# Optimization experiments

Hardware: AMD Instinct MI355X
Metric: run time of the kernel (lower is better)

## Reference

```python
import jax, jax.numpy as jnp
import numpy as np

EMBED_DIM = 512
B, N = 8, 2048


def setup_inputs() -> dict:
    key = jax.random.key(0)
    ks = jax.random.split(key, 9)
    d = EMBED_DIM
    s = 1.0 / np.sqrt(d)
    return {
        "x": jax.random.normal(ks[0], (B, N, d), dtype=jnp.float32),
        "Wq": jax.random.uniform(ks[1], (d, d), jnp.float32, -s, s),
        "bq": jax.random.uniform(ks[2], (d,), jnp.float32, -s, s),
        "Wk": jax.random.uniform(ks[3], (d, d), jnp.float32, -s, s),
        "bk": jax.random.uniform(ks[4], (d,), jnp.float32, -s, s),
        "Wv": jax.random.uniform(ks[5], (d, d), jnp.float32, -s, s),
        "bv": jax.random.uniform(ks[6], (d,), jnp.float32, -s, s),
        "Wo": jax.random.uniform(ks[7], (d, d), jnp.float32, -s, s),
        "bo": jax.random.uniform(ks[8], (d,), jnp.float32, -s, s),
    }


def reference(x, Wq, bq, Wk, bk, Wv, bv, Wo, bo):
    d = x.shape[-1]
    scale = d ** (-0.5)
    q = x @ Wq + bq              # [B, N, D]
    k = x @ Wk + bk
    v = x @ Wv + bv
    attn = jnp.einsum('bnd,bmd->bnm', q, k) * scale  # [B, N, N]
    attn = jax.nn.softmax(attn, axis=-1)
    out = jnp.einsum('bnm,bmd->bnd', attn, v)
    return out @ Wo + bo
```

## Files before the change

### kernel.cpp

```cpp
#include <hip/hip_runtime.h>
#include <hip/hip_bf16.h>
#include <hip/hip_fp8.h>
#include <stdint.h>

typedef __bf16 bf16;
typedef __attribute__((ext_vector_type(8))) short short8;
typedef __attribute__((ext_vector_type(4))) float f32x4;
typedef __attribute__((ext_vector_type(4))) bf16 bf16x4;
typedef __attribute__((ext_vector_type(8))) int int8v;
typedef __attribute__((ext_vector_type(4))) int int4v;

#define DIM 512
#define NBATCH 8
#define SEQ 2048

__device__ __forceinline__ void gld_lds16(const void* g, void* l) {
    __builtin_amdgcn_global_load_lds(
        (const __attribute__((address_space(1))) void*)g,
        (__attribute__((address_space(3))) void*)l,
        16, 0, 0);
}

__device__ __forceinline__ unsigned char f32_to_e4m3(float v) {
#if __has_builtin(__builtin_amdgcn_cvt_pk_fp8_f32)
    return (unsigned char)(__builtin_amdgcn_cvt_pk_fp8_f32(v, v, 0, false) & 0xff);
#else
    return __hip_cvt_float_to_fp8(v, __HIP_SATFINITE, __HIP_E4M3);
#endif
}

template <int MODE, int SWIZ>
__global__ __launch_bounds__(256) void gemm_bt(
    const bf16* __restrict__ A, const bf16* __restrict__ Bt,
    void* __restrict__ Cv, uint8_t* __restrict__ Vt,
    const float* __restrict__ bias, int N, int K, int gx)
{
    __shared__ bf16 smem[32768];
    bf16* Asb = smem;
    bf16* Bsb = smem + 16384;

    int bx, by;
    {
        const unsigned g = blockIdx.x;
        const unsigned xcd = g & 7;
        const unsigned t = g >> 3;
        const unsigned per = (gridDim.x >> 3) / (unsigned)gx;
        by = xcd * per + t / (unsigned)gx;
        bx = t % (unsigned)gx;
    }

    const int tid  = threadIdx.x;
    const int lane = tid & 63;
    const int w    = tid >> 6;
    const int wr   = w >> 1;
    const int wc   = w & 1;
    const int lm   = lane & 15;
    const int lk   = lane >> 4;
    const int fs   = lm & 7;
    const int rq   = tid >> 3;
    const int pc   = tid & 7;
    const int scol = ((pc ^ (rq & 7)) * 8);

    const bf16* Ag = A + (size_t)(by * 128) * K;
    const bf16* Bg = Bt + (size_t)(bx * 128) * K;

    f32x4 acc[4][4];
#pragma unroll
    for (int i = 0; i < 4; ++i)
#pragma unroll
        for (int j = 0; j < 4; ++j)
            acc[i][j] = (f32x4){0.f, 0.f, 0.f, 0.f};

    auto stage = [&](int kb, int buf) {
#pragma unroll
        for (int t = 0; t < 4; ++t) {
            const int r = t * 32 + rq;
            gld_lds16(Ag + (size_t)r * K + kb + scol,
                      Asb + buf * 8192 + t * 2048 + tid * 8);
            gld_lds16(Bg + (size_t)r * K + kb + scol,
                      Bsb + buf * 8192 + t * 2048 + tid * 8);
        }
    };
    auto compute = [&](int buf) {
        const bf16* Ab = Asb + buf * 8192;
        const bf16* Bb = Bsb + buf * 8192;
#pragma unroll
        for (int s = 0; s < 2; ++s) {
            const int u = ((s * 4 + lk) ^ fs) * 8;
            short8 fa[4], fb[4];
#pragma unroll
            for (int i = 0; i < 4; ++i)
                fa[i] = *(const short8*)&Ab[(wr * 64 + i * 16 + lm) * 64 + u];
#pragma unroll
            for (int j = 0; j < 4; ++j)
                fb[j] = *(const short8*)&Bb[(wc * 64 + j * 16 + lm) * 64 + u];
#pragma unroll
            for (int i = 0; i < 4; ++i)
#pragma unroll
                for (int j = 0; j < 4; ++j)
                    acc[i][j] = __builtin_amdgcn_mfma_f32_16x16x32_bf16(
                        fa[i], fb[j], acc[i][j], 0, 0, 0);
        }
    };

    stage(0, 0);
    __syncthreads();
    const int E = K >> 6;
#pragma unroll 2
    for (int e = 0; e < E; ++e) {
        if (e + 1 < E) stage((e + 1) << 6, (e + 1) & 1);
        compute(e & 1);
        __syncthreads();
    }

#pragma unroll
    for (int i = 0; i < 4; ++i)
#pragma unroll
        for (int j = 0; j < 4; ++j) {
            const int col = bx * 128 + wc * 64 + j * 16 + lm;
            const float bv = bias[col];
#pragma unroll
            for (int r = 0; r < 4; ++r)
                acc[i][j][r] += bv;
        }

    if (MODE == 2) {
        float* ft = (float*)smem;
        float* outp = (float*)Cv;
#pragma unroll
        for (int h = 0; h < 2; ++h) {
            if (wr == h) {
#pragma unroll
                for (int i = 0; i < 4; ++i)
#pragma unroll
                    for (int j = 0; j < 4; ++j)
#pragma unroll
                        for (int r = 0; r < 4; ++r)
                            ft[(i * 16 + lk * 4 + r) * 132 + wc * 64 + j * 16 + lm] =
                                acc[i][j][r];
            }
            __syncthreads();
            const int rr = tid >> 5, cc = (tid & 31) * 4;
#pragma unroll
            for (int p = 0; p < 8; ++p) {
                const int row = p * 8 + rr;
                *(float4*)&outp[(size_t)(by * 128 + h * 64 + row) * N +
                                bx * 128 + cc] = *(const float4*)&ft[row * 132 + cc];
            }
            __syncthreads();
        }
        return;
    }

    const int sub  = (bx * 128) >> 9;
    const int col0 = (bx * 128) & 511;

    if (sub == 2) {
        const int b  = (by * 128) >> 11;
        const int n0 = (by * 128) & 2047;
        uint8_t* t8 = (uint8_t*)smem;
#pragma unroll
        for (int i = 0; i < 4; ++i)
#pragma unroll
            for (int j = 0; j < 4; ++j)
#pragma unroll
                for (int r = 0; r < 4; ++r) {
                    const int fl = wc * 64 + j * 16 + lm;
                    const int nl = wr * 64 + i * 16 + lk * 4 + r;
                    t8[fl * 144 + nl] = f32_to_e4m3(32.0f * acc[i][j][r]);
                }
        __syncthreads();
        const int f = tid >> 1, nh = (tid & 1) * 64;
#pragma unroll
        for (int p = 0; p < 4; ++p) {
            const uint4 raw = *(const uint4*)&t8[f * 144 + nh + p * 16];
            *(uint4*)&Vt[((size_t)(b * 512 + col0 + f)) * 2048 +
                         n0 + nh + p * 16] = raw;
        }
        return;
    }

    uint8_t* d8 = (uint8_t*)Cv + (size_t)sub * 8388608;
    uint8_t* t8 = (uint8_t*)smem;
#pragma unroll
    for (int h = 0; h < 2; ++h) {
        if (wr == h) {
#pragma unroll
            for (int i = 0; i < 4; ++i)
#pragma unroll
                for (int j = 0; j < 4; ++j)
#pragma unroll
                    for (int r = 0; r < 4; ++r)
                        t8[(i * 16 + lk * 4 + r) * 144 + wc * 64 + j * 16 + lm] =
                            f32_to_e4m3(32.0f * acc[i][j][r]);
        }
        __syncthreads();
        const int rr = tid >> 3, cc = (tid & 7) * 16;
#pragma unroll
        for (int p = 0; p < 2; ++p) {
            const int row = p * 32 + rr;
            const uint4 raw = *(const uint4*)&t8[row * 144 + cc];
            *(uint4*)&d8[(size_t)(by * 128 + h * 64 + row) * 512 + col0 + cc] =
                raw;
        }
        __syncthreads();
    }
}

template <int MODE>
__global__ __launch_bounds__(256) void gemm_mx(
    const uint8_t* __restrict__ A, const uint8_t* __restrict__ Bt,
    void* __restrict__ Cv, float* __restrict__ rsum,
    int N, int K, long long sA, long long sB, long long sC, float alpha,
    int gx)
{
    __shared__ uint8_t smem[65536];
    uint8_t* Asb = smem;
    uint8_t* Bsb = smem + 32768;

    int bx, by, bz;
    {
        const unsigned g = blockIdx.x;
        bz = g & 7;
        const unsigned r = g >> 3;
        bx = r % (unsigned)gx;
        by = r / (unsigned)gx;
    }

    const int tid  = threadIdx.x;
    const int lane = tid & 63;
    const int w    = tid >> 6;
    const int wr   = w >> 1;
    const int wc   = w & 1;
    const int lm   = lane & 15;
    const int lk   = lane >> 4;
    const int rq   = tid >> 3;
    const int pc   = tid & 7;
    const int ssrc = (pc ^ (rq & 7)) * 16;
    const int ca   = ((2 * lk) ^ (lm & 7)) * 16;
    const int cb   = ((2 * lk + 1) ^ (lm & 7)) * 16;

    const size_t z = bz;
    const uint8_t* Ag = A + z * (size_t)sA + (size_t)(by * 128) * K;
    const uint8_t* Bg = Bt + z * (size_t)sB + (size_t)(bx * 128) * K;

    f32x4 acc[4][4];
#pragma unroll
    for (int i = 0; i < 4; ++i)
#pragma unroll
        for (int j = 0; j < 4; ++j)
            acc[i][j] = (f32x4){0.f, 0.f, 0.f, 0.f};

    auto stage = [&](int kb, int buf) {
#pragma unroll
        for (int t = 0; t < 4; ++t) {
            const int r = t * 32 + rq;
            gld_lds16(Ag + (size_t)r * K + kb + ssrc,
                      Asb + buf * 16384 + t * 4096 + tid * 16);
            gld_lds16(Bg + (size_t)r * K + kb + ssrc,
                      Bsb + buf * 16384 + t * 4096 + tid * 16);
        }
    };
    auto compute = [&](int buf) {
        const uint8_t* As = Asb + buf * 16384;
        const uint8_t* Bs = Bsb + buf * 16384;
        int8v fa[4];
#pragma unroll
        for (int i = 0; i < 4; ++i) {
            const uint8_t* rp = As + (wr * 64 + i * 16 + lm) * 128;
            const int4v lo = *(const int4v*)(rp + ca);
            const int4v hi = *(const int4v*)(rp + cb);
            fa[i] = (int8v){lo[0], lo[1], lo[2], lo[3], hi[0], hi[1], hi[2], hi[3]};
        }
#pragma unroll
        for (int j = 0; j < 4; ++j) {
            const uint8_t* rp = Bs + (wc * 64 + j * 16 + lm) * 128;
            const int4v lo = *(const int4v*)(rp + ca);
            const int4v hi = *(const int4v*)(rp + cb);
            const int8v fb = (int8v){lo[0], lo[1], lo[2], lo[3],
                                     hi[0], hi[1], hi[2], hi[3]};
#pragma unroll
            for (int i = 0; i < 4; ++i)
                acc[i][j] = __builtin_amdgcn_mfma_scale_f32_16x16x128_f8f6f4(
                    fa[i], fb, acc[i][j], 0, 0, 0, 127, 0, 127);
        }
    };

    stage(0, 0);
    __syncthreads();
    const int E = K >> 7;
#pragma unroll 2
    for (int e = 0; e < E; ++e) {
        if (e + 1 < E) stage((e + 1) << 7, (e + 1) & 1);
        compute(e & 1);
        __syncthreads();
    }

    const int orow0 = by * 128 + wr * 64;

    if (MODE == 4) {
#pragma unroll
        for (int i = 0; i < 4; ++i) {
            float psum[4] = {0.f, 0.f, 0.f, 0.f};
#pragma unroll
            for (int j = 0; j < 4; ++j)
#pragma unroll
                for (int r = 0; r < 4; ++r) {
                    const float e = __expf(acc[i][j][r] * alpha);
                    acc[i][j][r] = e;
                    psum[r] += e;
                }
#pragma unroll
            for (int m = 1; m < 16; m <<= 1)
#pragma unroll
                for (int r = 0; r < 4; ++r) psum[r] += __shfl_xor(psum[r], m);
            if (lm == 0) {
#pragma unroll
                for (int r = 0; r < 4; ++r)
                    atomicAdd(&rsum[z * SEQ + orow0 + i * 16 + lk * 4 + r],
                              psum[r]);
            }
        }
        uint8_t* dst = (uint8_t*)Cv + z * (size_t)sC;
#pragma unroll
        for (int h = 0; h < 2; ++h) {
            if (wr == h) {
#pragma unroll
                for (int i = 0; i < 4; ++i)
#pragma unroll
                    for (int j = 0; j < 4; ++j)
#pragma unroll
                        for (int r = 0; r < 4; ++r)
                            smem[(i * 16 + lk * 4 + r) * 144 +
                                 wc * 64 + j * 16 + lm] =
                                f32_to_e4m3(acc[i][j][r]);
            }
            __syncthreads();
            const int rr = tid >> 3, cc = (tid & 7) * 16;
#pragma unroll
            for (int p = 0; p < 2; ++p) {
                const int row = p * 32 + rr;
                const uint4 raw = *(const uint4*)&smem[row * 144 + cc];
                *(uint4*)&dst[(size_t)(by * 128 + h * 64 + row) * N +
                              bx * 128 + cc] = raw;
            }
            __syncthreads();
        }
        return;
    }

#pragma unroll
    for (int i = 0; i < 4; ++i) {
        float inv[4];
#pragma unroll
        for (int r = 0; r < 4; ++r)
            inv[r] = 1.0f / (32.0f * rsum[z * SEQ + orow0 + i * 16 + lk * 4 + r]);
#pragma unroll
        for (int j = 0; j < 4; ++j)
#pragma unroll
            for (int r = 0; r < 4; ++r)
                acc[i][j][r] *= inv[r];
    }
    bf16* dst = (bf16*)Cv + z * (size_t)sC;
    bf16* tile = (bf16*)smem;
#pragma unroll
    for (int h = 0; h < 2; ++h) {
        if (wr == h) {
#pragma unroll
            for (int i = 0; i < 4; ++i)
#pragma unroll
                for (int j = 0; j < 4; ++j)
#pragma unroll
                    for (int r = 0; r < 4; ++r)
                        tile[(i * 16 + lk * 4 + r) * 136 + wc * 64 + j * 16 + lm] =
                            (bf16)acc[i][j][r];
        }
        __syncthreads();
        const int rr0 = tid >> 4, cc = (tid & 15) * 8;
#pragma unroll
        for (int p = 0; p < 4; ++p) {
            const int row = p * 16 + rr0;
            const uint4 raw = *(const uint4*)&tile[row * 136 + cc];
            *(uint4*)&dst[(size_t)(by * 128 + h * 64 + row) * N + bx * 128 + cc] =
                raw;
        }
        __syncthreads();
    }
}

__global__ __launch_bounds__(256) void cvt_f32_bf16(
    const float* __restrict__ x, bf16* __restrict__ o, int n4)
{
    const int i = blockIdx.x * 256 + threadIdx.x;
    if (i >= n4) return;
    const float4 v = ((const float4*)x)[i];
    bf16x4 b;
    b[0] = (bf16)v.x; b[1] = (bf16)v.y; b[2] = (bf16)v.z; b[3] = (bf16)v.w;
    ((bf16x4*)o)[i] = b;
}

__global__ __launch_bounds__(256) void transpose4(
    const float* __restrict__ Wq, const float* __restrict__ Wk,
    const float* __restrict__ Wv, const float* __restrict__ Wo,
    bf16* __restrict__ Wcat, bf16* __restrict__ Wto,
    const float* __restrict__ bq, const float* __restrict__ bk,
    const float* __restrict__ bv, float* __restrict__ bcat,
    float* __restrict__ rowsum)
{
    const int widx = blockIdx.z;
    const int t0 = threadIdx.x;
    if (widx == 4) {
        const int idx = (blockIdx.y * 8 + blockIdx.x) * 256 + t0;
        rowsum[idx] = 0.0f;
        if (idx < 1536)
            bcat[idx] = (idx < 512) ? bq[idx]
                      : (idx < 1024) ? bk[idx - 512] : bv[idx - 1024];
        return;
    }
    __shared__ bf16 tile[64][65];
    const float* W = (widx == 0) ? Wq : (widx == 1) ? Wk : (widx == 2) ? Wv : Wo;
    bf16* dst = (widx < 3) ? (Wcat + (size_t)widx * 512 * 512) : Wto;
    const int tx = blockIdx.x, ty = blockIdx.y;
#pragma unroll
    for (int it = 0; it < 16; ++it) {
        const int e = it * 256 + t0;
        const int r = e >> 6, c = e & 63;
        tile[r][c] = (bf16)W[(size_t)(ty * 64 + r) * 512 + tx * 64 + c];
    }
    __syncthreads();
#pragma unroll
    for (int it = 0; it < 16; ++it) {
        const int e = it * 256 + t0;
        const int o = e >> 6, i = e & 63;
        dst[(size_t)(tx * 64 + o) * 512 + ty * 64 + i] = tile[i][o];
    }
}

extern "C" void kernel_launch(void* const* d_in, const int* in_sizes, int n_in,
                              void* d_out, int out_size, void* d_ws, size_t ws_size,
                              hipStream_t stream)
{
    const float* x  = (const float*)d_in[0];
    const float* Wq = (const float*)d_in[1];
    const float* bq = (const float*)d_in[2];
    const float* Wk = (const float*)d_in[3];
    const float* bk = (const float*)d_in[4];
    const float* Wv = (const float*)d_in[5];
    const float* bv = (const float*)d_in[6];
    const float* Wo = (const float*)d_in[7];
    const float* bo = (const float*)d_in[8];
    float* out = (float*)d_out;

    char* ws = (char*)d_ws;
    bf16*    Xb     = (bf16*)(ws);
    bf16*    Ctx    = (bf16*)(ws);
    bf16*    Wcat   = (bf16*)(ws + 16777216);
    bf16*    Wto    = (bf16*)(ws + 18350080);
    float*   bcat   = (float*)(ws + 18874368);
    float*   rowsum = (float*)(ws + 18880512);
    uint8_t* Q8     = (uint8_t*)(ws + 20971520);
    uint8_t* K8     = (uint8_t*)(ws + 29360128);
    uint8_t* Vt8    = (uint8_t*)(ws + 54525952);
    uint8_t* S8     = (uint8_t*)(ws + 62914560);

    transpose4<<<dim3(8, 8, 5), 256, 0, stream>>>(
        Wq, Wk, Wv, Wo, Wcat, Wto, bq, bk, bv, bcat, rowsum);
    cvt_f32_bf16<<<8192, 256, 0, stream>>>(x, Xb, 2097152);

    const float scale = 0.044194173824159216f;

    gemm_bt<3, 2><<<1536, 256, 0, stream>>>(
        Xb, Wcat, Q8, Vt8, bcat, 1536, 512, 12);

    gemm_mx<4><<<2048, 256, 0, stream>>>(
        Q8, K8, S8, rowsum, 2048, 512,
        2048LL * 512, 2048LL * 512, 2048LL * 2048, scale / 1024.0f, 16);

    gemm_mx<5><<<512, 256, 0, stream>>>(
        S8, Vt8, Ctx, rowsum, 512, 2048,
        2048LL * 2048, 512LL * 2048, 2048LL * 512, 1.0f, 4);

    gemm_bt<2, 2><<<512, 256, 0, stream>>>(
        Ctx, Wto, out, nullptr, bo, 512, 512, 4);
}
```

Before: 216.2 us.

## Split MX GEMM B staging with fine-grained vmcnt waits and compile-time K loop

Restructures the fp8 MX GEMM main loop. The loop count becomes a template parameter so it fully unrolls. The next tile's loads are issued right after a barrier, and the B tile is staged in two halves with explicit vmcnt waits, so the first half of the MFMAs can start before all loads land. s_setprio raises wave priority around the MFMA blocks. The goal is to overlap global-to-LDS loads with compute and drop the full-tile wait per iteration. The cost is hand-written waitcnt counts that must stay correct, and a wait at the top of each iteration that relies on the in-flight load count.

```diff
diff --git a/kernel.cpp b/kernel.cpp
--- a/kernel.cpp
+++ b/kernel.cpp
@@ -13,6 +13,8 @@
 #define DIM 512
 #define NBATCH 8
 #define SEQ 2048
+
+#define VMCNT(N) asm volatile("s_waitcnt vmcnt(" #N ")" ::: "memory")
 
 __device__ __forceinline__ void gld_lds16(const void* g, void* l) {
     __builtin_amdgcn_global_load_lds(
@@ -207,7 +209,7 @@
     }
 }
 
-template <int MODE>
+template <int MODE, int E>
 __global__ __launch_bounds__(256) void gemm_mx(
     const uint8_t* __restrict__ A, const uint8_t* __restrict__ Bt,
     void* __restrict__ Cv, float* __restrict__ rsum,
@@ -251,50 +253,86 @@
         for (int j = 0; j < 4; ++j)
             acc[i][j] = (f32x4){0.f, 0.f, 0.f, 0.f};
 
-    auto stage = [&](int kb, int buf) {
+    auto stageA = [&](int kb, int buf) {
 #pragma unroll
         for (int t = 0; t < 4; ++t) {
             const int r = t * 32 + rq;
             gld_lds16(Ag + (size_t)r * K + kb + ssrc,
                       Asb + buf * 16384 + t * 4096 + tid * 16);
+        }
+    };
+    auto stageB02 = [&](int kb, int buf) {
+#pragma unroll
+        for (int t = 0; t < 4; t += 2) {
+            const int r = t * 32 + rq;
             gld_lds16(Bg + (size_t)r * K + kb + ssrc,
                       Bsb + buf * 16384 + t * 4096 + tid * 16);
         }
     };
-    auto compute = [&](int buf) {
-        const uint8_t* As = Asb + buf * 16384;
-        const uint8_t* Bs = Bsb + buf * 16384;
+    auto stageB13 = [&](int kb, int buf) {
+#pragma unroll
+        for (int t = 1; t < 4; t += 2) {
+            const int r = t * 32 + rq;
+            gld_lds16(Bg + (size_t)r * K + kb + ssrc,
+                      Bsb + buf * 16384 + t * 4096 + tid * 16);
+        }
+    };
+    auto loadB = [&](const uint8_t* Bs, int j) -> int8v {
+        const uint8_t* rp = Bs + (wc * 64 + j * 16 + lm) * 128;
+        const int4v lo = *(const int4v*)(rp + ca);
+        const int4v hi = *(const int4v*)(rp + cb);
+        return (int8v){lo[0], lo[1], lo[2], lo[3], hi[0], hi[1], hi[2], hi[3]};
+    };
+
+    stageA(0, 0); stageB02(0, 0); stageB13(0, 0);
+
+#pragma unroll
+    for (int e = 0; e < E; ++e) {
+        const int p = e & 1;
+        const uint8_t* As = Asb + p * 16384;
+        const uint8_t* Bs = Bsb + p * 16384;
+
+        VMCNT(2);
+        __builtin_amdgcn_s_barrier();
+        if (e + 1 < E) {
+            stageA((e + 1) * 128, p ^ 1);
+            stageB02((e + 1) * 128, p ^ 1);
+            stageB13((e + 1) * 128, p ^ 1);
+        }
         int8v fa[4];
 #pragma unroll
         for (int i = 0; i < 4; ++i) {
             const uint8_t* rp = As + (wr * 64 + i * 16 + lm) * 128;
             const int4v lo = *(const int4v*)(rp + ca);
             const int4v hi = *(const int4v*)(rp + cb);
-            fa[i] = (int8v){lo[0], lo[1], lo[2], lo[3], hi[0], hi[1], hi[2], hi[3]};
-        }
-#pragma unroll
-        for (int j = 0; j < 4; ++j) {
-            const uint8_t* rp = Bs + (wc * 64 + j * 16 + lm) * 128;
-            const int4v lo = *(const int4v*)(rp + ca);
-            const int4v hi = *(const int4v*)(rp + cb);
-            const int8v fb = (int8v){lo[0], lo[1], lo[2], lo[3],
-                                     hi[0], hi[1], hi[2], hi[3]};
+            fa[i] = (int8v){lo[0], lo[1], lo[2], lo[3],
+                            hi[0], hi[1], hi[2], hi[3]};
+        }
+        __builtin_amdgcn_s_setprio(1);
+#pragma unroll
+        for (int j = 0; j < 2; ++j) {
+            const int8v fb = loadB(Bs, j);
 #pragma unroll
             for (int i = 0; i < 4; ++i)
                 acc[i][j] = __builtin_amdgcn_mfma_scale_f32_16x16x128_f8f6f4(
                     fa[i], fb, acc[i][j], 0, 0, 0, 127, 0, 127);
         }
-    };
-
-    stage(0, 0);
+        __builtin_amdgcn_s_setprio(0);
+
+        if (e + 1 < E) { VMCNT(8); } else { VMCNT(0); }
+        __builtin_amdgcn_s_barrier();
+        __builtin_amdgcn_s_setprio(1);
+#pragma unroll
+        for (int j = 2; j < 4; ++j) {
+            const int8v fb = loadB(Bs, j);
+#pragma unroll
+            for (int i = 0; i < 4; ++i)
+                acc[i][j] = __builtin_amdgcn_mfma_scale_f32_16x16x128_f8f6f4(
+                    fa[i], fb, acc[i][j], 0, 0, 0, 127, 0, 127);
+        }
+        __builtin_amdgcn_s_setprio(0);
+    }
     __syncthreads();
-    const int E = K >> 7;
-#pragma unroll 2
-    for (int e = 0; e < E; ++e) {
-        if (e + 1 < E) stage((e + 1) << 7, (e + 1) & 1);
-        compute(e & 1);
-        __syncthreads();
-    }
 
     const int orow0 = by * 128 + wr * 64;
 
@@ -472,11 +510,11 @@
     gemm_bt<3, 2><<<1536, 256, 0, stream>>>(
         Xb, Wcat, Q8, Vt8, bcat, 1536, 512, 12);
 
-    gemm_mx<4><<<2048, 256, 0, stream>>>(
+    gemm_mx<4, 4><<<2048, 256, 0, stream>>>(
         Q8, K8, S8, rowsum, 2048, 512,
         2048LL * 512, 2048LL * 512, 2048LL * 2048, scale / 1024.0f, 16);
 
-    gemm_mx<5><<<512, 256, 0, stream>>>(
+    gemm_mx<5, 16><<<512, 256, 0, stream>>>(
         S8, Vt8, Ctx, rowsum, 512, 2048,
         2048LL * 2048, 512LL * 2048, 2048LL * 512, 1.0f, 4);
 
```

Measured after the change: 215.5 us. Within noise of the previous version (-0.3%).

## Rework GEMM pipelines with explicit waitcnt barriers, single-buffered A, and compile-time K loops

Applied to the files above, without the earlier changes.

Both GEMM kernels replace __syncthreads with raw s_barrier plus explicit vmcnt/lgkmcnt waits and raise wave priority around the MFMA section. This lets the next tile's global-to-LDS loads overlap compute. The fp8 gemm_mx kernel now single-buffers the A tile, loading A fragments into registers before prefetching the next stage, which cuts LDS from 64KB to 48KB to allow higher occupancy. Its K loop count also becomes a template parameter so the loop fully unrolls. The hand-tuned waitcnt values carry a risk of subtle races if they miscount outstanding loads.

```diff
diff --git a/kernel.cpp b/kernel.cpp
--- a/kernel.cpp
+++ b/kernel.cpp
@@ -13,6 +13,10 @@
 #define DIM 512
 #define NBATCH 8
 #define SEQ 2048
+
+#define VMCNT(N) asm volatile("s_waitcnt vmcnt(" #N ")" ::: "memory")
+#define LGKMCNT0 asm volatile("s_waitcnt lgkmcnt(0)" ::: "memory")
+#define CFENCE   asm volatile("" ::: "memory")
 
 __device__ __forceinline__ void gld_lds16(const void* g, void* l) {
     __builtin_amdgcn_global_load_lds(
@@ -104,14 +108,23 @@
     };
 
     stage(0, 0);
-    __syncthreads();
     const int E = K >> 6;
 #pragma unroll 2
     for (int e = 0; e < E; ++e) {
-        if (e + 1 < E) stage((e + 1) << 6, (e + 1) & 1);
-        compute(e & 1);
-        __syncthreads();
-    }
+        const int p = e & 1;
+        CFENCE;
+        __builtin_amdgcn_s_barrier();
+        CFENCE;
+        if (e + 1 < E) { stage((e + 1) << 6, p ^ 1); VMCNT(8); }
+        else           { VMCNT(0); }
+        CFENCE;
+        __builtin_amdgcn_s_barrier();
+        CFENCE;
+        __builtin_amdgcn_s_setprio(1);
+        compute(p);
+        __builtin_amdgcn_s_setprio(0);
+    }
+    __syncthreads();
 
 #pragma unroll
     for (int i = 0; i < 4; ++i)
@@ -207,16 +220,16 @@
     }
 }
 
-template <int MODE>
+template <int MODE, int E>
 __global__ __launch_bounds__(256) void gemm_mx(
     const uint8_t* __restrict__ A, const uint8_t* __restrict__ Bt,
     void* __restrict__ Cv, float* __restrict__ rsum,
     int N, int K, long long sA, long long sB, long long sC, float alpha,
     int gx)
 {
-    __shared__ uint8_t smem[65536];
-    uint8_t* Asb = smem;
-    uint8_t* Bsb = smem + 32768;
+    __shared__ uint8_t smem[49152];
+    uint8_t* Ab  = smem;
+    uint8_t* Bsb = smem + 16384;
 
     int bx, by, bz;
     {
@@ -251,27 +264,47 @@
         for (int j = 0; j < 4; ++j)
             acc[i][j] = (f32x4){0.f, 0.f, 0.f, 0.f};
 
-    auto stage = [&](int kb, int buf) {
+    auto stageA = [&](int kb) {
 #pragma unroll
         for (int t = 0; t < 4; ++t) {
             const int r = t * 32 + rq;
             gld_lds16(Ag + (size_t)r * K + kb + ssrc,
-                      Asb + buf * 16384 + t * 4096 + tid * 16);
+                      Ab + t * 4096 + tid * 16);
+        }
+    };
+    auto stageB = [&](int kb, int buf) {
+#pragma unroll
+        for (int t = 0; t < 4; ++t) {
+            const int r = t * 32 + rq;
             gld_lds16(Bg + (size_t)r * K + kb + ssrc,
                       Bsb + buf * 16384 + t * 4096 + tid * 16);
         }
     };
-    auto compute = [&](int buf) {
-        const uint8_t* As = Asb + buf * 16384;
-        const uint8_t* Bs = Bsb + buf * 16384;
+
+    stageA(0); stageB(0, 0);
+
+#pragma unroll
+    for (int e = 0; e < E; ++e) {
+        const int p = e & 1;
+        VMCNT(0);
+        __builtin_amdgcn_s_barrier();
+        CFENCE;
         int8v fa[4];
 #pragma unroll
         for (int i = 0; i < 4; ++i) {
-            const uint8_t* rp = As + (wr * 64 + i * 16 + lm) * 128;
+            const uint8_t* rp = Ab + (wr * 64 + i * 16 + lm) * 128;
             const int4v lo = *(const int4v*)(rp + ca);
             const int4v hi = *(const int4v*)(rp + cb);
-            fa[i] = (int8v){lo[0], lo[1], lo[2], lo[3], hi[0], hi[1], hi[2], hi[3]};
-        }
+            fa[i] = (int8v){lo[0], lo[1], lo[2], lo[3],
+                            hi[0], hi[1], hi[2], hi[3]};
+        }
+        LGKMCNT0;
+        __builtin_amdgcn_sched_barrier(0);
+        __builtin_amdgcn_s_barrier();
+        CFENCE;
+        if (e + 1 < E) { stageA((e + 1) * 128); stageB((e + 1) * 128, p ^ 1); }
+        const uint8_t* Bs = Bsb + p * 16384;
+        __builtin_amdgcn_s_setprio(1);
 #pragma unroll
         for (int j = 0; j < 4; ++j) {
             const uint8_t* rp = Bs + (wc * 64 + j * 16 + lm) * 128;
@@ -284,17 +317,9 @@
                 acc[i][j] = __builtin_amdgcn_mfma_scale_f32_16x16x128_f8f6f4(
                     fa[i], fb, acc[i][j], 0, 0, 0, 127, 0, 127);
         }
-    };
-
-    stage(0, 0);
+        __builtin_amdgcn_s_setprio(0);
+    }
     __syncthreads();
-    const int E = K >> 7;
-#pragma unroll 2
-    for (int e = 0; e < E; ++e) {
-        if (e + 1 < E) stage((e + 1) << 7, (e + 1) & 1);
-        compute(e & 1);
-        __syncthreads();
-    }
 
     const int orow0 = by * 128 + wr * 64;
 
@@ -472,11 +497,11 @@
     gemm_bt<3, 2><<<1536, 256, 0, stream>>>(
         Xb, Wcat, Q8, Vt8, bcat, 1536, 512, 12);
 
-    gemm_mx<4><<<2048, 256, 0, stream>>>(
+    gemm_mx<4, 4><<<2048, 256, 0, stream>>>(
         Q8, K8, S8, rowsum, 2048, 512,
         2048LL * 512, 2048LL * 512, 2048LL * 2048, scale / 1024.0f, 16);
 
-    gemm_mx<5><<<512, 256, 0, stream>>>(
+    gemm_mx<5, 16><<<512, 256, 0, stream>>>(
         S8, Vt8, Ctx, rowsum, 512, 2048,
         2048LL * 2048, 512LL * 2048, 2048LL * 512, 1.0f, 4);
 
```

Result: no change. 212.6 us (-1.7%).
